# Kernel tuning notes

Hardware: AMD Instinct MI355X
Metric: run time of the kernel (lower is better)

## Reference

```python
import jax, jax.numpy as jnp
import numpy as np

N, IN, OUT = 8192, 4096, 4096
GROUP = 4
ACT_BITS = 8


def setup_inputs() -> dict:
    key = jax.random.key(0)
    k_x, k_w, k_b = jax.random.split(key, 3)
    input = jax.random.normal(k_x, (N, IN), dtype=jnp.float32)
    # ternary weights in {-1, 0, +1}, stored as float for compute
    weight = jax.random.randint(k_w, (OUT, IN), -1, 2).astype(jnp.float32)
    weight_scale = jnp.ones((1,), dtype=jnp.float32) * 0.02
    bias = jax.random.normal(k_b, (OUT,), dtype=jnp.float32) * 0.01
    return {"input": input, "weight": weight, "weight_scale": weight_scale, "bias": bias}


def reference(input, weight, weight_scale, bias):
    n, in_f = input.shape
    out_f = weight.shape[0]
    qmax = 2 ** (ACT_BITS - 1) - 1  # 127
    # absmax activation quantization (inference path)
    act_scale = jnp.abs(input).max() / qmax
    x_q = jnp.clip(jnp.round(input / act_scale), -(qmax + 1), qmax)
    # LUT path math: per 4-wide group, contribution = sum(w_group) * mean(x_group)
    g = in_f // GROUP
    x_mean = x_q.reshape(n, g, GROUP).mean(axis=-1)          # [N, G]
    w_sum = weight.reshape(out_f, g, GROUP).sum(axis=-1)     # [OUT, G]
    out = jnp.einsum('ng,og->no', x_mean, w_sum)
    out = out * weight_scale * act_scale + bias
    return out
```

## Files before the change

### kernel.cpp

```cpp
#include <hip/hip_runtime.h>

#define NROWS 8192
#define INF   4096
#define OUTF  4096
#define G     1024

typedef _Float16 f16x8 __attribute__((ext_vector_type(8)));
typedef float    f32x4 __attribute__((ext_vector_type(4)));


__global__ void pass1(const float4* __restrict__ x,
                      const float4* __restrict__ w,
                      float* __restrict__ partial,
                      _Float16* __restrict__ ws) {
    const int t = threadIdx.x;
    const int b = blockIdx.x;
    if (b < 2048) {
        const int stride = 2048 * 256;
        int i = b * 256 + t;
        float m = 0.f;
        #pragma unroll 4
        for (int it = 0; it < 16; ++it, i += stride) {
            float4 v = x[i];
            m = fmaxf(m, fmaxf(fmaxf(fabsf(v.x), fabsf(v.y)),
                               fmaxf(fabsf(v.z), fabsf(v.w))));
        }
        for (int off = 32; off; off >>= 1)
            m = fmaxf(m, __shfl_down(m, off));
        __shared__ float wm[4];
        int lane = t & 63, wave = t >> 6;
        if (lane == 0) wm[wave] = m;
        __syncthreads();
        if (t == 0)
            partial[b] = fmaxf(fmaxf(wm[0], wm[1]), fmaxf(wm[2], wm[3]));
    } else {
        int i = (b - 2048) * 4096 + t;
        #pragma unroll 4
        for (int it = 0; it < 16; ++it, i += 256) {
            float4 v = w[i];
            ws[i] = (_Float16)(v.x + v.y + v.z + v.w);
        }
    }
}

__global__ void absmax_final(const float* __restrict__ partial,
                             const float* __restrict__ wscale,
                             float* __restrict__ sc) {
    int t = threadIdx.x;
    float m = 0.f;
    #pragma unroll
    for (int u = 0; u < 8; ++u)
        m = fmaxf(m, partial[t + u * 256]);
    for (int off = 32; off; off >>= 1)
        m = fmaxf(m, __shfl_down(m, off));
    __shared__ float wm[4];
    int lane = t & 63, wave = t >> 6;
    if (lane == 0) wm[wave] = m;
    __syncthreads();
    if (t == 0) {
        float bm = fmaxf(fmaxf(wm[0], wm[1]), fmaxf(wm[2], wm[3]));
        float s = bm * (1.0f / 127.0f);
        sc[0] = s;
        sc[1] = 127.0f / bm;
        sc[2] = s * 0.25f * wscale[0];
    }
}

__global__ void xquant(const float4* __restrict__ x,
                       const float* __restrict__ sc,
                       _Float16* __restrict__ xs) {
    const float inv = sc[1];
    int i0 = blockIdx.x * 512 + threadIdx.x;
    #pragma unroll
    for (int u = 0; u < 2; ++u) {
        int i = i0 + u * 256;
        float4 v = x[i];
        xs[i] = (_Float16)(rintf(v.x * inv) + rintf(v.y * inv) +
                           rintf(v.z * inv) + rintf(v.w * inv));
    }
}

#define BM 256
#define BN 128
#define BK 32

__device__ __forceinline__ void async_copy16(const void* g, void* l) {
    __builtin_amdgcn_global_load_lds(
        (const __attribute__((address_space(1))) unsigned int*)g,
        (__attribute__((address_space(3))) unsigned int*)l,
        16, 0, 0);
}

__global__ __launch_bounds__(256, 2) void gemm_kernel(
    const _Float16* __restrict__ A,
    const _Float16* __restrict__ B,
    const float* __restrict__ bias,
    const float* __restrict__ sc,
    float* __restrict__ out) {

    __shared__ alignas(16) _Float16 As[2][BM * BK];
    __shared__ alignas(16) _Float16 Bs[2][BN * BK];

    const int t = threadIdx.x;
    const int lane = t & 63;
    const int wave = t >> 6;
    const int wm = (wave >> 1) * 128;
    const int wn = (wave & 1) * 64;

    const long rowA0 = (long)blockIdx.y * BM;
    const long rowB0 = (long)blockIdx.x * BN;

    f32x4 acc[8][4] = {};

    const int srow = lane >> 2;
    const int scol = ((lane & 3) << 3) ^ (((lane >> 3) & 3) << 3);
    const int swzR = ((lane >> 1) & 3) << 3;

    auto stage = [&](int buf, int k0) {
        #pragma unroll
        for (int i = 0; i < 6; ++i) {
            const int c = wave * 6 + i;
            if (c < 16) {
                const int row = c * 16 + srow;
                async_copy16(A + (rowA0 + row) * (long)G + k0 + scol, &As[buf][c * 512]);
            } else {
                const int row = (c - 16) * 16 + srow;
                async_copy16(B + (rowB0 + row) * (long)G + k0 + scol, &Bs[buf][(c - 16) * 512]);
            }
        }
    };

    stage(0, 0);
    __syncthreads();

    int cur = 0;
    for (int ks = 0; ks < G / BK; ++ks) {
        if (ks + 1 < G / BK) stage(cur ^ 1, (ks + 1) * BK);

        f16x8 af[8], bf[4];
        #pragma unroll
        for (int mi = 0; mi < 8; ++mi)
            af[mi] = *(const f16x8*)&As[cur][(wm + mi * 16 + (lane & 15)) * BK
                                            + (((lane >> 4) * 8) ^ swzR)];
        #pragma unroll
        for (int nj = 0; nj < 4; ++nj)
            bf[nj] = *(const f16x8*)&Bs[cur][(wn + nj * 16 + (lane & 15)) * BK
                                            + (((lane >> 4) * 8) ^ swzR)];

        #pragma unroll
        for (int mi = 0; mi < 8; ++mi)
            #pragma unroll
            for (int nj = 0; nj < 4; ++nj)
                acc[mi][nj] = __builtin_amdgcn_mfma_f32_16x16x32_f16(
                    af[mi], bf[nj], acc[mi][nj], 0, 0, 0);

        __syncthreads();
        cur ^= 1;
    }

    const float scale = sc[2];
    const int r0 = (int)rowA0 + wm + (lane >> 4) * 4;
    const int c0 = (int)rowB0 + wn + (lane & 15);
    #pragma unroll
    for (int nj = 0; nj < 4; ++nj) {
        const int col = c0 + nj * 16;
        const float b = bias[col];
        #pragma unroll
        for (int mi = 0; mi < 8; ++mi) {
            const int row = r0 + mi * 16;
            #pragma unroll
            for (int r = 0; r < 4; ++r)
                out[(long)(row + r) * OUTF + col] = acc[mi][nj][r] * scale + b;
        }
    }
}

extern "C" void kernel_launch(void* const* d_in, const int* in_sizes, int n_in,
                              void* d_out, int out_size, void* d_ws, size_t ws_size,
                              hipStream_t stream) {
    const float* input  = (const float*)d_in[0];
    const float* weight = (const float*)d_in[1];
    const float* wscale = (const float*)d_in[2];
    const float* bias   = (const float*)d_in[3];
    float* out = (float*)d_out;

    float* scales   = (float*)d_ws;
    float* partials = (float*)((char*)d_ws + 16);
    _Float16* x_sum = (_Float16*)((char*)d_ws + 8208);
    _Float16* w_sum = (_Float16*)((char*)d_ws + 8208 + (size_t)NROWS * G * 2);

    pass1<<<3072, 256, 0, stream>>>((const float4*)input, (const float4*)weight,
                                    partials, w_sum);
    absmax_final<<<1, 256, 0, stream>>>(partials, wscale, scales);
    xquant<<<16384, 256, 0, stream>>>((const float4*)input, scales, x_sum);
    gemm_kernel<<<dim3(OUTF / BN, NROWS / BM), 256, 0, stream>>>(
        x_sum, w_sum, bias, scales, out);
}
```

Measured before the change: 386.5 us.

## Split preprocessing kernels, fold final absmax into xquant, widen per-thread loads

The combined pass1 kernel is split into a separate absmax partial-reduction kernel and a weight group-sum kernel. The single-block absmax_final launch is removed: every xquant block now re-reduces the 2048 partials itself to derive the scale, and block 0 writes the scale values for the GEMM. Each thread loads 8 float4s with more loads in flight and writes a packed 8-wide f16 vector instead of scalar halfs. This removes one serial launch and issues wider stores, at the cost of redundant partial reads in every xquant block.

```diff
diff --git a/kernel.cpp b/kernel.cpp
--- a/kernel.cpp
+++ b/kernel.cpp
@@ -9,44 +9,55 @@
 typedef float    f32x4 __attribute__((ext_vector_type(4)));
 
 
-__global__ void pass1(const float4* __restrict__ x,
-                      const float4* __restrict__ w,
-                      float* __restrict__ partial,
-                      _Float16* __restrict__ ws) {
+__global__ void absmax_part(const float4* __restrict__ x,
+                            float* __restrict__ partial) {
     const int t = threadIdx.x;
-    const int b = blockIdx.x;
-    if (b < 2048) {
-        const int stride = 2048 * 256;
-        int i = b * 256 + t;
-        float m = 0.f;
-        #pragma unroll 4
-        for (int it = 0; it < 16; ++it, i += stride) {
-            float4 v = x[i];
-            m = fmaxf(m, fmaxf(fmaxf(fabsf(v.x), fabsf(v.y)),
-                               fmaxf(fabsf(v.z), fabsf(v.w))));
-        }
-        for (int off = 32; off; off >>= 1)
-            m = fmaxf(m, __shfl_down(m, off));
-        __shared__ float wm[4];
-        int lane = t & 63, wave = t >> 6;
-        if (lane == 0) wm[wave] = m;
-        __syncthreads();
-        if (t == 0)
-            partial[b] = fmaxf(fmaxf(wm[0], wm[1]), fmaxf(wm[2], wm[3]));
-    } else {
-        int i = (b - 2048) * 4096 + t;
-        #pragma unroll 4
-        for (int it = 0; it < 16; ++it, i += 256) {
-            float4 v = w[i];
-            ws[i] = (_Float16)(v.x + v.y + v.z + v.w);
-        }
-    }
-}
-
-__global__ void absmax_final(const float* __restrict__ partial,
-                             const float* __restrict__ wscale,
-                             float* __restrict__ sc) {
-    int t = threadIdx.x;
+    const long base = (long)blockIdx.x * 4096 + t;
+    float m[8] = {0.f, 0.f, 0.f, 0.f, 0.f, 0.f, 0.f, 0.f};
+    #pragma unroll
+    for (int batch = 0; batch < 2; ++batch) {
+        float4 v[8];
+        #pragma unroll
+        for (int k = 0; k < 8; ++k)
+            v[k] = x[base + batch * 2048 + k * 256];
+        #pragma unroll
+        for (int k = 0; k < 8; ++k)
+            m[k] = fmaxf(m[k], fmaxf(fmaxf(fabsf(v[k].x), fabsf(v[k].y)),
+                                     fmaxf(fabsf(v[k].z), fabsf(v[k].w))));
+    }
+    float mm = 0.f;
+    #pragma unroll
+    for (int k = 0; k < 8; ++k) mm = fmaxf(mm, m[k]);
+    for (int off = 32; off; off >>= 1)
+        mm = fmaxf(mm, __shfl_down(mm, off));
+    __shared__ float wm[4];
+    const int lane = t & 63, wave = t >> 6;
+    if (lane == 0) wm[wave] = mm;
+    __syncthreads();
+    if (t == 0)
+        partial[blockIdx.x] = fmaxf(fmaxf(wm[0], wm[1]), fmaxf(wm[2], wm[3]));
+}
+
+__global__ void wsum_kernel(const float* __restrict__ w,
+                            _Float16* __restrict__ ws) {
+    const long g0 = (long)blockIdx.x * 2048 + (long)threadIdx.x * 8;
+    f32x4 v[8];
+    #pragma unroll
+    for (int j = 0; j < 8; ++j)
+        v[j] = *(const f32x4*)(w + (g0 + j) * 4);
+    f16x8 r;
+    #pragma unroll
+    for (int j = 0; j < 8; ++j)
+        r[j] = (_Float16)(v[j][0] + v[j][1] + v[j][2] + v[j][3]);
+    *(f16x8*)(ws + g0) = r;
+}
+
+__global__ void xquant(const float* __restrict__ x,
+                       const float* __restrict__ partial,
+                       const float* __restrict__ wscale,
+                       float* __restrict__ sc,
+                       _Float16* __restrict__ xs) {
+    const int t = threadIdx.x;
     float m = 0.f;
     #pragma unroll
     for (int u = 0; u < 8; ++u)
@@ -54,30 +65,27 @@
     for (int off = 32; off; off >>= 1)
         m = fmaxf(m, __shfl_down(m, off));
     __shared__ float wm[4];
-    int lane = t & 63, wave = t >> 6;
+    const int lane = t & 63, wave = t >> 6;
     if (lane == 0) wm[wave] = m;
     __syncthreads();
-    if (t == 0) {
-        float bm = fmaxf(fmaxf(wm[0], wm[1]), fmaxf(wm[2], wm[3]));
+    const float bm = fmaxf(fmaxf(wm[0], wm[1]), fmaxf(wm[2], wm[3]));
+    const float inv = 127.0f / bm;
+    if (blockIdx.x == 0 && t == 0) {
         float s = bm * (1.0f / 127.0f);
         sc[0] = s;
-        sc[1] = 127.0f / bm;
         sc[2] = s * 0.25f * wscale[0];
     }
-}
-
-__global__ void xquant(const float4* __restrict__ x,
-                       const float* __restrict__ sc,
-                       _Float16* __restrict__ xs) {
-    const float inv = sc[1];
-    int i0 = blockIdx.x * 512 + threadIdx.x;
-    #pragma unroll
-    for (int u = 0; u < 2; ++u) {
-        int i = i0 + u * 256;
-        float4 v = x[i];
-        xs[i] = (_Float16)(rintf(v.x * inv) + rintf(v.y * inv) +
-                           rintf(v.z * inv) + rintf(v.w * inv));
-    }
+    const long g0 = (long)blockIdx.x * 2048 + (long)t * 8;
+    f32x4 v[8];
+    #pragma unroll
+    for (int j = 0; j < 8; ++j)
+        v[j] = *(const f32x4*)(x + (g0 + j) * 4);
+    f16x8 r;
+    #pragma unroll
+    for (int j = 0; j < 8; ++j)
+        r[j] = (_Float16)(rintf(v[j][0] * inv) + rintf(v[j][1] * inv) +
+                          rintf(v[j][2] * inv) + rintf(v[j][3] * inv));
+    *(f16x8*)(xs + g0) = r;
 }
 
 #define BM 256
@@ -189,10 +197,9 @@
     _Float16* x_sum = (_Float16*)((char*)d_ws + 8208);
     _Float16* w_sum = (_Float16*)((char*)d_ws + 8208 + (size_t)NROWS * G * 2);
 
-    pass1<<<3072, 256, 0, stream>>>((const float4*)input, (const float4*)weight,
-                                    partials, w_sum);
-    absmax_final<<<1, 256, 0, stream>>>(partials, wscale, scales);
-    xquant<<<16384, 256, 0, stream>>>((const float4*)input, scales, x_sum);
+    absmax_part<<<2048, 256, 0, stream>>>((const float4*)input, partials);
+    wsum_kernel<<<2048, 256, 0, stream>>>(weight, w_sum);
+    xquant<<<4096, 256, 0, stream>>>(input, partials, wscale, scales, x_sum);
     gemm_kernel<<<dim3(OUTF / BN, NROWS / BM), 256, 0, stream>>>(
         x_sum, w_sum, bias, scales, out);
 }
```

New measurement: 389.7 us. No clear change (+0.8%).
